# Kernel tuning notes

Measured on AMD Instinct MI355X. Metric: run time of the kernel, lower is better.

## Reference

```python
import jax, jax.numpy as jnp
import numpy as np

BLOCK = 16                      # NVFP4 block size along K
FP4_MAX = 6.0                   # e2m1 max magnitude
FP8_MAX = 448.0                 # e4m3 max
E2M1_GRID = jnp.array([0.0, 0.5, 1.0, 1.5, 2.0, 3.0, 4.0, 5.0, 6.0], dtype=jnp.float32)
E2M1_MIDS = jnp.array([0.25, 0.75, 1.25, 1.75, 2.5, 3.5, 4.5, 5.5], dtype=jnp.float32)


def _global_sf(t):
    # 448*6 / amax(|t|), amax clamped to 1e-12 (matches torch code)
    amax = jnp.clip(jnp.max(jnp.abs(jnp.nan_to_num(t))), 1e-12, None)
    return (FP8_MAX * FP4_MAX) / amax


def _round_e4m3(v):
    # round-to-nearest e4m3fn via dtype cast
    return v.astype(jnp.float8_e4m3fn).astype(jnp.float32)


def _round_e2m1(v):
    # nearest value on the signed e2m1 grid, clamped to +-6
    a = jnp.clip(jnp.abs(v), 0.0, FP4_MAX)
    idx = jnp.searchsorted(E2M1_MIDS, a)
    return E2M1_GRID[idx] * jnp.sign(v)


def nvfp4_quant_dequant(t, global_sf):
    """Simulate nvfp4_quantize + dequant. Returns t_hat ~= t * global_sf
    (values representable as e2m1 * e4m3 block scale)."""
    rows, K = t.shape
    tb = t.reshape(rows, K // BLOCK, BLOCK)
    amax = jnp.max(jnp.abs(tb), axis=-1, keepdims=True)            # [rows, K/16, 1]
    sf = _round_e4m3(jnp.clip(amax * global_sf / FP4_MAX, 0.0, FP8_MAX))
    inv_sf = jnp.where(sf > 0, global_sf / sf, 0.0)
    q = _round_e2m1(tb * inv_sf)                                   # fp4 codes (as f32)
    return (q * sf).reshape(rows, K)                               # dequant in scaled space


def setup_inputs() -> dict:
    key = jax.random.key(0)
    kx, kw = jax.random.split(key)
    M, K, N = 4096, 4096, 4096
    x = jax.random.normal(kx, (M, K), dtype=jnp.float32)
    w = jax.random.normal(kw, (N, K), dtype=jnp.float32)
    return {"x": x, "w": w}


def reference(x, w):
    w_gsf = _global_sf(w)
    x_gsf = _global_sf(x)
    w_hat = nvfp4_quant_dequant(w, w_gsf)   # ~= w * w_gsf
    x_hat = nvfp4_quant_dequant(x, x_gsf)   # ~= x * x_gsf
    alpha = 1.0 / (w_gsf * x_gsf)
    # mm_fp4: (x_q xsf) @ (w_q wsf)^T * alpha  -> [M, N]
    return jnp.einsum('mk,nk->mn', x_hat, w_hat) * alpha
```

## Files before the change

### kernel.cpp

```cpp
#include <hip/hip_runtime.h>
#include <hip/hip_bf16.h>
#include <stdint.h>

#define M_DIM 4096
#define N_DIM 4096
#define K_DIM 4096
#define KB 8192

typedef __bf16 bf16x8 __attribute__((ext_vector_type(8)));
typedef float  f32x4  __attribute__((ext_vector_type(4)));

__global__ __launch_bounds__(256) void amax2_kernel(const float* __restrict__ x,
                                                    const float* __restrict__ w,
                                                    unsigned int* __restrict__ out) {
    __shared__ float red[4];
    const int half = blockIdx.x >> 10;
    const float4* in4 = (const float4*)(half ? w : x);
    const int lid = (blockIdx.x & 1023) * 256 + threadIdx.x;
    const int S = 1024 * 256;
    float m0 = 0.f, m1 = 0.f, m2 = 0.f, m3 = 0.f;
#pragma unroll
    for (int k = 0; k < 4; ++k) {
        float4 a = in4[lid + (4 * k + 0) * S];
        float4 b = in4[lid + (4 * k + 1) * S];
        float4 c = in4[lid + (4 * k + 2) * S];
        float4 d = in4[lid + (4 * k + 3) * S];
        m0 = fmaxf(m0, fmaxf(fmaxf(fabsf(a.x), fabsf(a.y)), fmaxf(fabsf(a.z), fabsf(a.w))));
        m1 = fmaxf(m1, fmaxf(fmaxf(fabsf(b.x), fabsf(b.y)), fmaxf(fabsf(b.z), fabsf(b.w))));
        m2 = fmaxf(m2, fmaxf(fmaxf(fabsf(c.x), fabsf(c.y)), fmaxf(fabsf(c.z), fabsf(c.w))));
        m3 = fmaxf(m3, fmaxf(fmaxf(fabsf(d.x), fabsf(d.y)), fmaxf(fabsf(d.z), fabsf(d.w))));
    }
    float m = fmaxf(fmaxf(m0, m1), fmaxf(m2, m3));
#pragma unroll
    for (int off = 32; off > 0; off >>= 1)
        m = fmaxf(m, __shfl_xor(m, off, 64));
    if ((threadIdx.x & 63) == 0) red[threadIdx.x >> 6] = m;
    __syncthreads();
    if (threadIdx.x == 0) {
        float r = fmaxf(fmaxf(red[0], red[1]), fmaxf(red[2], red[3]));
        atomicMax(out + half, __float_as_uint(r));
    }
}

__device__ __forceinline__ float round_e4m3(float v) {
    if (!(v > 0.f)) return 0.f;
    uint32_t u = __float_as_uint(v);
    int e = (int)(u >> 23) - 127;
    if (e < -6) e = -6;
    float ulp     = __uint_as_float((uint32_t)(e - 3 + 127) << 23);
    float inv_ulp = __uint_as_float((uint32_t)(3 - e + 127) << 23);
    return rintf(v * inv_ulp) * ulp;
}

__device__ __forceinline__ float round_e2m1_mag(float a) {
    float q = 0.f;
    q = (a > 0.25f) ? 0.5f : q;
    q = (a > 0.75f) ? 1.0f : q;
    q = (a > 1.25f) ? 1.5f : q;
    q = (a > 1.75f) ? 2.0f : q;
    q = (a > 2.5f)  ? 3.0f : q;
    q = (a > 3.5f)  ? 4.0f : q;
    q = (a > 4.5f)  ? 5.0f : q;
    q = (a > 5.5f)  ? 6.0f : q;
    return q;
}

__device__ __forceinline__ unsigned int pack2(float va, float vb, float inv, float sf) {
    float xa = va * inv, xb = vb * inv;
    float qa = round_e2m1_mag(fminf(fabsf(xa), 6.f));
    float qb = round_e2m1_mag(fminf(fabsf(xb), 6.f));
    float ta = copysignf(qa, xa) * sf;
    float tb = copysignf(qb, xb) * sf;
    return (__float_as_uint(ta) >> 16) | ((__float_as_uint(tb) >> 16) << 16);
}

__global__ __launch_bounds__(256) void quant2_kernel(const float* __restrict__ x,
                                                     const float* __restrict__ w,
                                                     unsigned short* __restrict__ xq,
                                                     unsigned short* __restrict__ wq,
                                                     const unsigned int* __restrict__ amax_bits) {
    const float gx = 2688.0f / fmaxf(__uint_as_float(amax_bits[0]), 1e-12f);
    const float gw = 2688.0f / fmaxf(__uint_as_float(amax_bits[1]), 1e-12f);
    const int t0 = blockIdx.x * 256 + threadIdx.x;
    const int S = 4096 * 256;
#pragma unroll
    for (int it = 0; it < 8; ++it) {
        const bool isx = (it < 4);
        const float4* src = (const float4*)(isx ? x : w);
        unsigned short* dst = isx ? xq : wq;
        const float gsf = isx ? gx : gw;
        const int li = t0 + (isx ? it : it - 4) * S;
        float4 v = src[li];
        float am = fmaxf(fmaxf(fabsf(v.x), fabsf(v.y)), fmaxf(fabsf(v.z), fabsf(v.w)));
        am = fmaxf(am, __shfl_xor(am, 1, 64));
        am = fmaxf(am, __shfl_xor(am, 2, 64));
        float sf  = round_e4m3(fminf(fmaxf(am * gsf / 6.0f, 0.f), 448.0f));
        float inv = (sf > 0.f) ? (gsf / sf) : 0.f;
        uint2 o;
        o.x = pack2(v.x, v.y, inv, sf);
        o.y = pack2(v.z, v.w, inv, sf);
        *(uint2*)(dst + (size_t)li * 4) = o;
    }
}

__global__ __launch_bounds__(512, 2) void gemm_kernel(const unsigned short* __restrict__ A,
                                                      const unsigned short* __restrict__ B,
                                                      float* __restrict__ C,
                                                      const unsigned int* __restrict__ amax_bits) {
    __shared__ alignas(16) char smem[131072];

    const int tid  = threadIdx.x;
    const int lane = tid & 63;
    const int wid  = tid >> 6;
    const int wr   = wid >> 2;
    const int wc   = wid & 3;

    int bid = blockIdx.x;
    int swz = (bid & 7) * 32 + (bid >> 3);
    const int brow = (swz >> 4) * 256;
    const int bcol = (swz & 15) * 256;

    int rowS[2], colS[2], Lr[2];
#pragma unroll
    for (int r = 0; r < 2; ++r) {
        int L = r * 8192 + tid * 16;
        int b = L ^ (((L >> 7) & 7) << 4);
        Lr[r] = L;
        rowS[r] = b >> 7;
        colS[r] = b & 127;
    }
    const char* Abase = (const char*)A;
    const char* Bbase = (const char*)B;

    auto STAGE = [&](int ts, int slot) {
        const char* mat = (slot >= 2) ? Abase : Bbase;
        int rbase = ((slot >= 2) ? brow : bcol) + ((slot & 1) ? 128 : 0);
        int loff  = (ts & 1) * 65536 + ((slot >= 2) ? 0 : 32768) + ((slot & 1) ? 16384 : 0);
#pragma unroll
        for (int r = 0; r < 2; ++r) {
            const char* gp = mat + (size_t)(rbase + rowS[r]) * KB + ts * 128 + colS[r];
            __builtin_amdgcn_global_load_lds(
                (const __attribute__((address_space(1))) unsigned int*)gp,
                (__attribute__((address_space(3))) unsigned int*)(smem + loff + Lr[r]),
                16, 0, 0);
        }
    };

    const int lr  = lane & 15;
    const int kg  = lane >> 4;
    const int swx = (lr & 7) << 4;
    int colA[2];
#pragma unroll
    for (int ks = 0; ks < 2; ++ks) colA[ks] = (ks * 64 + kg * 16) ^ swx;
    int rowAb[8], rowBb[4];
#pragma unroll
    for (int m = 0; m < 8; ++m) rowAb[m] = (wr * 128 + m * 16 + lr) * 128;
#pragma unroll
    for (int n = 0; n < 4; ++n) rowBb[n] = 32768 + (wc * 64 + n * 16 + lr) * 128;

    bf16x8 bR[4][2];
    bf16x8 aS0[2][2], aS1[2][2];
    f32x4  acc[8][4];
#pragma unroll
    for (int m = 0; m < 8; ++m)
#pragma unroll
        for (int n = 0; n < 4; ++n)
#pragma unroll
            for (int j = 0; j < 4; ++j) acc[m][n][j] = 0.f;

    auto LDB_ALL = [&](int bufo) {
#pragma unroll
        for (int n = 0; n < 4; ++n)
#pragma unroll
            for (int ks = 0; ks < 2; ++ks)
                bR[n][ks] = *(const bf16x8*)(smem + bufo + rowBb[n] + colA[ks]);
    };
    auto LDC = [&](int bufo, int ci, bf16x8 (&s)[2][2]) {
#pragma unroll
        for (int mm = 0; mm < 2; ++mm)
#pragma unroll
            for (int ks = 0; ks < 2; ++ks)
                s[mm][ks] = *(const bf16x8*)(smem + bufo + rowAb[ci * 2 + mm] + colA[ks]);
    };
    auto MMAc = [&](int ci, bf16x8 (&s)[2][2]) {
        __builtin_amdgcn_s_setprio(1);
#pragma unroll
        for (int ks = 0; ks < 2; ++ks)
#pragma unroll
            for (int mm = 0; mm < 2; ++mm)
#pragma unroll
                for (int n = 0; n < 4; ++n)
                    acc[ci * 2 + mm][n] =
                        __builtin_amdgcn_mfma_f32_16x16x32_bf16(s[mm][ks], bR[n][ks], acc[ci * 2 + mm][n], 0, 0, 0);
        __builtin_amdgcn_s_setprio(0);
    };

    STAGE(0, 0); STAGE(0, 1); STAGE(0, 2); STAGE(0, 3);
    asm volatile("s_waitcnt vmcnt(4)" ::: "memory");
    STAGE(1, 0); STAGE(1, 1); STAGE(1, 2);
    asm volatile("s_waitcnt vmcnt(6)" ::: "memory");
    __builtin_amdgcn_s_barrier();
    LDC(0, 0, aS0); LDB_ALL(0); STAGE(1, 3);
    __builtin_amdgcn_s_barrier();

#pragma unroll 1
    for (int i = 0; i < 32; ++i) {
        int e = 2 * i;
        int n2 = (e + 2 < 64) ? e + 2 : 63;
        int n3 = (e + 3 < 64) ? e + 3 : 63;

        LDC(0, 1, aS1); MMAc(0, aS0); STAGE(n2, 0);
        __builtin_amdgcn_s_barrier();
        LDC(0, 2, aS0); MMAc(1, aS1); STAGE(n2, 1);
        __builtin_amdgcn_s_barrier();
        LDC(0, 3, aS1); MMAc(2, aS0); STAGE(n2, 2);
        asm volatile("s_waitcnt vmcnt(6)" ::: "memory");
        __builtin_amdgcn_s_barrier();
        LDC(65536, 0, aS0); MMAc(3, aS1); LDB_ALL(65536); STAGE(n2, 3);
        __builtin_amdgcn_s_barrier();
        LDC(65536, 1, aS1); MMAc(0, aS0); STAGE(n3, 0);
        __builtin_amdgcn_s_barrier();
        LDC(65536, 2, aS0); MMAc(1, aS1); STAGE(n3, 1);
        __builtin_amdgcn_s_barrier();
        LDC(65536, 3, aS1); MMAc(2, aS0); STAGE(n3, 2);
        asm volatile("s_waitcnt vmcnt(6)" ::: "memory");
        __builtin_amdgcn_s_barrier();
        LDC(0, 0, aS0); MMAc(3, aS1); LDB_ALL(0); STAGE(n3, 3);
        __builtin_amdgcn_s_barrier();
    }

    float ax = fmaxf(__uint_as_float(amax_bits[0]), 1e-12f);
    float aw = fmaxf(__uint_as_float(amax_bits[1]), 1e-12f);
    float alpha = 1.0f / ((2688.0f / ax) * (2688.0f / aw));
    const int r4 = kg * 4;
    const int cn = lane & 15;
#pragma unroll
    for (int m = 0; m < 8; ++m)
#pragma unroll
        for (int n = 0; n < 4; ++n)
#pragma unroll
            for (int j = 0; j < 4; ++j) {
                int row = brow + wr * 128 + m * 16 + r4 + j;
                int col = bcol + wc * 64 + n * 16 + cn;
                C[(size_t)row * N_DIM + col] = acc[m][n][j] * alpha;
            }
}

extern "C" void kernel_launch(void* const* d_in, const int* in_sizes, int n_in,
                              void* d_out, int out_size, void* d_ws, size_t ws_size,
                              hipStream_t stream) {
    const float* x = (const float*)d_in[0];
    const float* w = (const float*)d_in[1];
    float* out = (float*)d_out;

    unsigned int*   amax  = (unsigned int*)d_ws;
    unsigned short* x_hat = (unsigned short*)((char*)d_ws + 256);
    unsigned short* w_hat = x_hat + (size_t)M_DIM * K_DIM;

    hipMemsetAsync(d_ws, 0, 256, stream);

    hipLaunchKernelGGL(amax2_kernel, dim3(2048), dim3(256), 0, stream, x, w, amax);
    hipLaunchKernelGGL(quant2_kernel, dim3(4096), dim3(256), 0, stream, x, w, x_hat, w_hat,
                       (const unsigned int*)amax);
    hipLaunchKernelGGL(gemm_kernel, dim3(256), dim3(512), 0, stream,
                       x_hat, w_hat, out, (const unsigned int*)d_ws);
}
```

Measured before the change: 174.0 us.

## Restructure GEMM main loop into quadrant-based LDS loads with explicit lgkm waits

Replaces the per-row-chunk LDS fragment loading (A in 2-row chunks, all of B at once) with a quadrant schedule. Each tile step loads half of A and half of B, then runs four 4x2 MFMA quadrants, reusing each register fragment across more MFMAs. Explicit lgkmcnt waits and barriers are inserted around each quadrant. The intent is to cut LDS read traffic per MFMA and change register pressure. It risks exposing LDS latency, because loads are no longer overlapped with the preceding MFMA block, and it adds more barriers.

```diff
diff --git a/kernel.cpp b/kernel.cpp
--- a/kernel.cpp
+++ b/kernel.cpp
@@ -158,8 +158,8 @@
 #pragma unroll
     for (int n = 0; n < 4; ++n) rowBb[n] = 32768 + (wc * 64 + n * 16 + lr) * 128;
 
-    bf16x8 bR[4][2];
-    bf16x8 aS0[2][2], aS1[2][2];
+    bf16x8 aH[4][2];
+    bf16x8 bH0[2][2], bH1[2][2];
     f32x4  acc[8][4];
 #pragma unroll
     for (int m = 0; m < 8; ++m)
@@ -168,66 +168,73 @@
 #pragma unroll
             for (int j = 0; j < 4; ++j) acc[m][n][j] = 0.f;
 
-    auto LDB_ALL = [&](int bufo) {
-#pragma unroll
-        for (int n = 0; n < 4; ++n)
+    auto LDA_H = [&](int bufo, int mh) {
+#pragma unroll
+        for (int mm = 0; mm < 4; ++mm)
 #pragma unroll
             for (int ks = 0; ks < 2; ++ks)
-                bR[n][ks] = *(const bf16x8*)(smem + bufo + rowBb[n] + colA[ks]);
-    };
-    auto LDC = [&](int bufo, int ci, bf16x8 (&s)[2][2]) {
-#pragma unroll
-        for (int mm = 0; mm < 2; ++mm)
+                aH[mm][ks] = *(const bf16x8*)(smem + bufo + rowAb[mh * 4 + mm] + colA[ks]);
+    };
+    auto LDB_H = [&](int bufo, bf16x8 (&b)[2][2], int nh) {
+#pragma unroll
+        for (int nn = 0; nn < 2; ++nn)
 #pragma unroll
             for (int ks = 0; ks < 2; ++ks)
-                s[mm][ks] = *(const bf16x8*)(smem + bufo + rowAb[ci * 2 + mm] + colA[ks]);
-    };
-    auto MMAc = [&](int ci, bf16x8 (&s)[2][2]) {
+                b[nn][ks] = *(const bf16x8*)(smem + bufo + rowBb[nh * 2 + nn] + colA[ks]);
+    };
+    auto MMA_Q = [&](int mh, int nh, bf16x8 (&b)[2][2]) {
         __builtin_amdgcn_s_setprio(1);
 #pragma unroll
         for (int ks = 0; ks < 2; ++ks)
 #pragma unroll
-            for (int mm = 0; mm < 2; ++mm)
-#pragma unroll
-                for (int n = 0; n < 4; ++n)
-                    acc[ci * 2 + mm][n] =
-                        __builtin_amdgcn_mfma_f32_16x16x32_bf16(s[mm][ks], bR[n][ks], acc[ci * 2 + mm][n], 0, 0, 0);
+            for (int mm = 0; mm < 4; ++mm)
+#pragma unroll
+                for (int nn = 0; nn < 2; ++nn) {
+                    int m = mh * 4 + mm, n = nh * 2 + nn;
+                    acc[m][n] = __builtin_amdgcn_mfma_f32_16x16x32_bf16(aH[mm][ks], b[nn][ks], acc[m][n], 0, 0, 0);
+                }
         __builtin_amdgcn_s_setprio(0);
+    };
+
+#define BAR()   __builtin_amdgcn_s_barrier()
+#define LGKM0() asm volatile("s_waitcnt lgkmcnt(0)" ::: "memory")
+#define LGKM8() asm volatile("s_waitcnt lgkmcnt(8)" ::: "memory")
+#define VM6()   asm volatile("s_waitcnt vmcnt(6)" ::: "memory")
+
+    auto TILE = [&](int bufo, int tl1, int tn) {
+        LDA_H(bufo, 0); LDB_H(bufo, bH0, 0); STAGE(tl1, 3);
+        LGKM8(); BAR(); LGKM0();
+        MMA_Q(0, 0, bH0); BAR();
+        LDB_H(bufo, bH1, 1); STAGE(tn, 0);
+        BAR(); LGKM0();
+        MMA_Q(0, 1, bH1); BAR();
+        LDA_H(bufo, 1); STAGE(tn, 1);
+        BAR(); LGKM0();
+        MMA_Q(1, 1, bH1); BAR();
+        STAGE(tn, 2);
+        VM6(); BAR();
+        MMA_Q(1, 0, bH0); BAR();
     };
 
     STAGE(0, 0); STAGE(0, 1); STAGE(0, 2); STAGE(0, 3);
     asm volatile("s_waitcnt vmcnt(4)" ::: "memory");
     STAGE(1, 0); STAGE(1, 1); STAGE(1, 2);
     asm volatile("s_waitcnt vmcnt(6)" ::: "memory");
-    __builtin_amdgcn_s_barrier();
-    LDC(0, 0, aS0); LDB_ALL(0); STAGE(1, 3);
-    __builtin_amdgcn_s_barrier();
+    BAR();
 
 #pragma unroll 1
     for (int i = 0; i < 32; ++i) {
         int e = 2 * i;
         int n2 = (e + 2 < 64) ? e + 2 : 63;
         int n3 = (e + 3 < 64) ? e + 3 : 63;
-
-        LDC(0, 1, aS1); MMAc(0, aS0); STAGE(n2, 0);
-        __builtin_amdgcn_s_barrier();
-        LDC(0, 2, aS0); MMAc(1, aS1); STAGE(n2, 1);
-        __builtin_amdgcn_s_barrier();
-        LDC(0, 3, aS1); MMAc(2, aS0); STAGE(n2, 2);
-        asm volatile("s_waitcnt vmcnt(6)" ::: "memory");
-        __builtin_amdgcn_s_barrier();
-        LDC(65536, 0, aS0); MMAc(3, aS1); LDB_ALL(65536); STAGE(n2, 3);
-        __builtin_amdgcn_s_barrier();
-        LDC(65536, 1, aS1); MMAc(0, aS0); STAGE(n3, 0);
-        __builtin_amdgcn_s_barrier();
-        LDC(65536, 2, aS0); MMAc(1, aS1); STAGE(n3, 1);
-        __builtin_amdgcn_s_barrier();
-        LDC(65536, 3, aS1); MMAc(2, aS0); STAGE(n3, 2);
-        asm volatile("s_waitcnt vmcnt(6)" ::: "memory");
-        __builtin_amdgcn_s_barrier();
-        LDC(0, 0, aS0); MMAc(3, aS1); LDB_ALL(0); STAGE(n3, 3);
-        __builtin_amdgcn_s_barrier();
-    }
+        TILE(0,     e + 1, n2);
+        TILE(65536, n2,    n3);
+    }
+
+#undef BAR
+#undef LGKM0
+#undef LGKM8
+#undef VM6
 
     float ax = fmaxf(__uint_as_float(amax_bits[0]), 1e-12f);
     float aw = fmaxf(__uint_as_float(amax_bits[1]), 1e-12f);
```

Result: slower. 179.8 us (+3.3%).
